# Kernel tuning notes

Hardware: AMD Instinct MI355X
Metric: run time of the kernel (lower is better)

## Reference

```python
import jax, jax.numpy as jnp
import numpy as np

NUM_CODEBOOKS = 4
CODEBOOK_SIZE = 4096
CODEBOOK_DIM = 512


def setup_inputs() -> dict:
    key = jax.random.key(0)
    k1, k2 = jax.random.split(key)
    inputs = jax.random.normal(k1, (8, 2048, CODEBOOK_DIM), dtype=jnp.float32)
    # nn.init.uniform_(codebook.weight, -1/codebook_size, 1/codebook_size)
    bound = 1.0 / CODEBOOK_SIZE
    codebook = jax.random.uniform(k2, (CODEBOOK_SIZE, CODEBOOK_DIM),
                                  dtype=jnp.float32, minval=-bound, maxval=bound)
    return {"inputs": inputs, "codebook": codebook}


def reference(inputs, codebook):
    original_shape = inputs.shape
    x = inputs.reshape(-1, CODEBOOK_DIM)  # [N, D]
    cb_sq = jnp.sum(codebook ** 2, axis=1)  # [K]

    def stage(residual, _):
        # distances: ||r||^2 - 2 r.W^T + ||w||^2  -> [N, K]
        distances = (jnp.sum(residual ** 2, axis=1, keepdims=True)
                     - 2.0 * residual @ codebook.T
                     + cb_sq[None, :])
        indices = jnp.argmin(distances, axis=-1)  # [N]
        # one-hot matmul in torch == gather; same math
        quantized = codebook[indices]  # [N, D]
        # straight-through estimator
        q_ste = residual + jax.lax.stop_gradient(quantized - residual)
        new_residual = residual - q_ste
        return new_residual, (q_ste, indices)

    _, (q_stages, idx_stages) = jax.lax.scan(stage, x, None, length=NUM_CODEBOOKS)
    quantized_out = jnp.sum(q_stages, axis=0).reshape(original_shape)
    # all_indices stacked along last dim: [B, T, num_codebooks]
    all_indices = jnp.moveaxis(idx_stages, 0, -1).reshape(*original_shape[:-1], NUM_CODEBOOKS)
    vq_loss = jnp.float32(0.0)  # eval mode: self.training is False
    return quantized_out, all_indices, vq_loss
```

## Files before the change

kernel.cpp:

```cpp
#include <hip/hip_runtime.h>
#include <math.h>


namespace {
constexpr int N_ROWS     = 16384;
constexpr int DIM        = 512;
constexpr int K_CODES    = 4096;
constexpr int NUM_STAGES = 4;

constexpr int KTILES = 32;
constexpr int LTS    = 72;
constexpr float EPS  = 1e-3f;
constexpr int CAP    = 2;

constexpr int CROWS  = 32;
constexpr int CGRIDY = 8;
constexpr int WSTRC  = 68;
constexpr int RSTR   = 68;

constexpr size_t Q_OFF    = 0;
constexpr size_t IDX_OFF  = (size_t)N_ROWS * DIM;
constexpr size_t LOSS_OFF = IDX_OFF + (size_t)N_ROWS * NUM_STAGES;

constexpr size_t RES_OFF  = 0;
constexpr size_t RH_OFF   = (size_t)N_ROWS * DIM * 4;
constexpr size_t WH_OFF   = RH_OFF + (size_t)N_ROWS * DIM * 2;
constexpr size_t CBSQ_OFF = WH_OFF + (size_t)K_CODES * DIM * 2;
constexpr size_t RSQ_OFF  = CBSQ_OFF + (size_t)K_CODES * 4;
constexpr size_t PART_OFF = RSQ_OFF + (size_t)N_ROWS * 4;
constexpr size_t GBUF_OFF = PART_OFF + (size_t)N_ROWS * KTILES * 4;
constexpr size_t BCNT_OFF = GBUF_OFF + (size_t)N_ROWS * KTILES * CAP * 8;
constexpr size_t BENT_OFF = BCNT_OFF + 128;
constexpr size_t BEST_OFF = BENT_OFF + (size_t)KTILES * N_ROWS * 4;

constexpr unsigned long long EMPTY_E = 0xFFFFFFFFFFFFFFFFull;
constexpr unsigned long long OVFL_E  = 0xFFFFFFFFFFFFFFFEull;
}

typedef short bf16x8 __attribute__((ext_vector_type(8)));
typedef float f32x4  __attribute__((ext_vector_type(4)));

__device__ __forceinline__ unsigned short f2bf(float x) {
    unsigned int u = __float_as_uint(x);
    return (unsigned short)((u + 0x7fffu + ((u >> 16) & 1u)) >> 16);
}

__device__ __forceinline__ float f4c(const float4& v, int q) {
    return q == 0 ? v.x : q == 1 ? v.y : q == 2 ? v.z : v.w;
}

__device__ __forceinline__ float rowsq_tree(const float v8[8], int lane) {
#pragma clang fp contract(off)
    float P[4];
#pragma unroll
    for (int b = 0; b < 4; ++b) {
        float xa = v8[2 * b];
        float xb = v8[2 * b + 1];
        float sa = xa * xa;
        float sb = xb * xb;
        float R  = sa + sb;
        float t  = R + __shfl_down(R, 16, 64);
        float u  = t + __shfl_down(t, 32, 64);
        float a  = u + __shfl_down(u, 8, 64);
        float c  = a + __shfl_down(a, 4, 64);
        float d  = c + __shfl_down(c, 2, 64);
        P[b]     = d + __shfl_down(d, 1, 64);
    }
    float s01 = P[0] + P[1];
    float s23 = P[2] + P[3];
    return s01 + s23;
}

__global__ __launch_bounds__(64)
void cbsq_wh_kernel(const float* __restrict__ cb, float* __restrict__ cb_sq,
                    unsigned short* __restrict__ wh, float* __restrict__ loss) {
    int k = blockIdx.x;
    int lane = threadIdx.x;
    const float* row = cb + (size_t)k * DIM;
    unsigned short* whp = wh + (size_t)k * DIM;
    float v8[8];
#pragma unroll
    for (int i = 0; i < 8; ++i) {
        float v = row[lane + i * 64];
        v8[i] = v;
        whp[lane + i * 64] = f2bf(v);
    }
    float s = rowsq_tree(v8, lane);
    if (lane == 0) cb_sq[k] = s;
    if (k == 0 && lane == 0) *loss = 0.0f;
}

__global__ __launch_bounds__(256)
void init_kernel(const float* __restrict__ input,
                 unsigned short* __restrict__ rh,
                 float* __restrict__ rsq, int* __restrict__ bcnt) {
    const int t = threadIdx.x;
    if (blockIdx.x == 0 && t < KTILES) bcnt[t] = 0;
    const int lane = t & 63;
    const int sub  = t >> 6;
    const int row  = blockIdx.x * 4 + sub;
    const float* x = input + (size_t)row * DIM;
    unsigned short* rhp = rh + (size_t)row * DIM;
    float v8[8];
#pragma unroll
    for (int i = 0; i < 8; ++i) {
        int d = lane + i * 64;
        float v = x[d];
        v8[i] = v;
        rhp[d] = f2bf(v);
    }
    float s = rowsq_tree(v8, lane);
    if (lane == 0) rsq[row] = s;
}

__global__ __launch_bounds__(256, 2)
void passA_kernel(const unsigned short* __restrict__ rh,
                  const unsigned short* __restrict__ wh,
                  const float* __restrict__ cb_sq,
                  const float* __restrict__ rsq,
                  float* __restrict__ part,
                  unsigned long long* __restrict__ gbuf) {
    const int jb = blockIdx.x;
    const int mb = blockIdx.y;
    const int mbase = mb * 128;
    const int nbase = jb * 128;

    __shared__ __align__(16) unsigned short At[128 * LTS];
    __shared__ __align__(16) unsigned short Bt[128 * LTS];
    __shared__ float rowmin[128][2];

    const int t    = threadIdx.x;
    const int lane = t & 63;
    const int wid  = t >> 6;
    const int wr   = wid >> 1;
    const int wc   = wid & 1;

    f32x4 acc[4][4];
#pragma unroll
    for (int mi = 0; mi < 4; ++mi)
#pragma unroll
        for (int ni = 0; ni < 4; ++ni) acc[mi][ni] = (f32x4){0.f, 0.f, 0.f, 0.f};

    for (int k0 = 0; k0 < DIM; k0 += 64) {
#pragma unroll
        for (int p = 0; p < 4; ++p) {
            int idx = p * 256 + t;
            int row = idx >> 3;
            int d8  = idx & 7;
            uint4 va = *(const uint4*)(rh + (size_t)(mbase + row) * DIM + k0 + d8 * 8);
            *(uint4*)&At[row * LTS + d8 * 8] = va;
            uint4 vb = *(const uint4*)(wh + (size_t)(nbase + row) * DIM + k0 + d8 * 8);
            *(uint4*)&Bt[row * LTS + d8 * 8] = vb;
        }
        __syncthreads();

#pragma unroll
        for (int kk = 0; kk < 2; ++kk) {
            bf16x8 af[4], bfr[4];
#pragma unroll
            for (int mi = 0; mi < 4; ++mi)
                af[mi] = *(const bf16x8*)&At[(wr * 64 + mi * 16 + (lane & 15)) * LTS
                                             + kk * 32 + (lane >> 4) * 8];
#pragma unroll
            for (int ni = 0; ni < 4; ++ni)
                bfr[ni] = *(const bf16x8*)&Bt[(wc * 64 + ni * 16 + (lane & 15)) * LTS
                                              + kk * 32 + (lane >> 4) * 8];
#pragma unroll
            for (int mi = 0; mi < 4; ++mi)
#pragma unroll
                for (int ni = 0; ni < 4; ++ni)
                    acc[mi][ni] = __builtin_amdgcn_mfma_f32_16x16x32_bf16(
                        af[mi], bfr[ni], acc[mi][ni], 0, 0, 0);
        }
        __syncthreads();
    }

    int* scnt = (int*)Bt;
    unsigned long long* sbuf = (unsigned long long*)At;
    if (t < 128) {
        scnt[t] = 0;
        sbuf[t * CAP + 0] = EMPTY_E;
        sbuf[t * CAP + 1] = EMPTY_E;
    }

#pragma unroll
    for (int mi = 0; mi < 4; ++mi) {
#pragma unroll
        for (int reg = 0; reg < 4; ++reg) {
            int rloc = wr * 64 + mi * 16 + (lane >> 4) * 4 + reg;
            float rsqv = rsq[mbase + rloc];
            float m = INFINITY;
#pragma unroll
            for (int ni = 0; ni < 4; ++ni) {
                int kg = nbase + wc * 64 + ni * 16 + (lane & 15);
                float y;
                {
#pragma clang fp contract(off)
                    float t2 = 2.0f * acc[mi][ni][reg];
                    float u  = rsqv - t2;
                    y        = u + cb_sq[kg];
                }
                m = fminf(m, y);
            }
#pragma unroll
            for (int off = 1; off < 16; off <<= 1)
                m = fminf(m, __shfl_xor(m, off, 64));
            if ((lane & 15) == 0) rowmin[rloc][wc] = m;
        }
    }
    __syncthreads();

#pragma unroll
    for (int mi = 0; mi < 4; ++mi) {
#pragma unroll
        for (int reg = 0; reg < 4; ++reg) {
            int rloc = wr * 64 + mi * 16 + (lane >> 4) * 4 + reg;
            float thrT = fminf(rowmin[rloc][0], rowmin[rloc][1]) + EPS;
            float rsqv = rsq[mbase + rloc];
#pragma unroll
            for (int ni = 0; ni < 4; ++ni) {
                int kg = nbase + wc * 64 + ni * 16 + (lane & 15);
                float y;
                {
#pragma clang fp contract(off)
                    float t2 = 2.0f * acc[mi][ni][reg];
                    float u  = rsqv - t2;
                    y        = u + cb_sq[kg];
                }
                if (y <= thrT) {
                    int pos = atomicAdd(&scnt[rloc], 1);
                    if (pos < CAP)
                        sbuf[rloc * CAP + pos] =
                            ((unsigned long long)__float_as_uint(y) << 32) |
                            (unsigned)kg;
                }
            }
        }
    }
    __syncthreads();

    if (t < 128) {
        part[(size_t)jb * N_ROWS + (mbase + t)] =
            fminf(rowmin[t][0], rowmin[t][1]);
        unsigned long long s0 = sbuf[t * CAP + 0];
        unsigned long long s1 = sbuf[t * CAP + 1];
        if (scnt[t] > CAP) s0 = OVFL_E;
        size_t bidx = ((size_t)jb * N_ROWS + (mbase + t)) * CAP;
        gbuf[bidx]     = s0;
        gbuf[bidx + 1] = s1;
    }
}

__global__ __launch_bounds__(256)
void passBC_kernel(const float* __restrict__ res,
                   const float* __restrict__ cb,
                   const float* __restrict__ cb_sq,
                   const float* __restrict__ rsq,
                   const float* __restrict__ part,
                   const unsigned long long* __restrict__ gbuf,
                   int* __restrict__ bcnt, int* __restrict__ bent,
                   unsigned long long* __restrict__ best) {
    const int t   = threadIdx.x;
    const int jr  = t & 31;
    const int rs  = t >> 5;
    const int row = blockIdx.x * 8 + rs;

    float pv = part[(size_t)jr * N_ROWS + row];
    float m = pv;
#pragma unroll
    for (int off = 1; off < 32; off <<= 1)
        m = fminf(m, __shfl_xor(m, off, 32));
    const float thr = m + EPS;

    float by = INFINITY; int bk = 0x7fffffff;

    if (pv <= thr) {
        size_t bidx = ((size_t)jr * N_ROWS + row) * CAP;
        unsigned long long s0 = gbuf[bidx];
        unsigned long long s1 = gbuf[bidx + 1];
        if (s0 == OVFL_E) {
            int pos = atomicAdd(&bcnt[jr], 1);
            bent[(size_t)jr * N_ROWS + pos] = row;
        } else {
            const float* rr  = res + (size_t)row * DIM;
            const float rsqv = rsq[row];
#pragma unroll
            for (int sl = 0; sl < CAP; ++sl) {
                unsigned long long s = sl ? s1 : s0;
                float yh = __uint_as_float((unsigned)(s >> 32));
                if (!(yh <= thr)) continue;
                int k = (int)(s & 0xFFFFFFFFull);
                const float* wp = cb + (size_t)k * DIM;
                float dot = 0.0f;
#pragma unroll 8
                for (int d = 0; d < DIM; d += 4) {
                    float4 r4 = *(const float4*)(rr + d);
                    float4 w4 = *(const float4*)(wp + d);
                    dot = fmaf(r4.x, w4.x, dot);
                    dot = fmaf(r4.y, w4.y, dot);
                    dot = fmaf(r4.z, w4.z, dot);
                    dot = fmaf(r4.w, w4.w, dot);
                }
                float y;
                {
#pragma clang fp contract(off)
                    float t2 = 2.0f * dot;
                    float u  = rsqv - t2;
                    y        = u + cb_sq[k];
                }
                if (y < by || (y == by && k < bk)) { by = y; bk = k; }
            }
        }
    }

    unsigned long long pk =
        ((unsigned long long)__float_as_uint(by) << 32) | (unsigned)bk;
#pragma unroll
    for (int off = 1; off < 32; off <<= 1) {
        unsigned long long o =
            (unsigned long long)__shfl_xor((long long)pk, off, 32);
        if (o < pk) pk = o;
    }
    if (jr == 0) best[row] = pk;
}

__global__ __launch_bounds__(256)
void passC_kernel(const float* __restrict__ res,
                  const float* __restrict__ cb,
                  const float* __restrict__ cb_sq,
                  const float* __restrict__ rsq,
                  const int* __restrict__ bcnt, const int* __restrict__ bent,
                  unsigned long long* __restrict__ best) {
    const int j   = blockIdx.x;
    const int cnt = bcnt[j];
    const int t   = threadIdx.x;
    const int cg  = t & 31;
    const int rg  = t >> 5;

    __shared__ __align__(16) float Ws[128 * WSTRC];
    __shared__ __align__(16) float Rs[CROWS * RSTR];
    __shared__ int   rowl[CROWS];
    __shared__ float rsql[CROWS];

    for (int base = blockIdx.y * CROWS; base < cnt; base += gridDim.y * CROWS) {
        if (t < CROWS) {
            int e  = base + t;
            int rw = bent[(size_t)j * N_ROWS + (e < cnt ? e : cnt - 1)];
            rowl[t] = rw;
            rsql[t] = rsq[rw];
        }
        __syncthreads();
        const int nrows = min(CROWS, cnt - base);

        float acc[4][4];
#pragma unroll
        for (int ri = 0; ri < 4; ++ri)
#pragma unroll
            for (int q = 0; q < 4; ++q) acc[ri][q] = 0.0f;

        for (int d0 = 0; d0 < DIM; d0 += 64) {
#pragma unroll
            for (int p = 0; p < 8; ++p) {
                int idx  = p * 256 + t;
                int cand = idx >> 4;
                int d4   = idx & 15;
                float4 v = *(const float4*)(cb + (size_t)(j * 128 + cand) * DIM + d0 + d4 * 4);
                int s = d4 ^ ((cand >> 2) & 7) ^ ((cand >> 5) & 3);
                *(float4*)&Ws[cand * WSTRC + s * 4] = v;
            }
#pragma unroll
            for (int p = 0; p < 2; ++p) {
                int idx = p * 256 + t;
                int row = idx >> 4;
                int d4  = idx & 15;
                float4 v = *(const float4*)(res + (size_t)rowl[row] * DIM + d0 + d4 * 4);
                *(float4*)&Rs[row * RSTR + d4 * 4] = v;
            }
            __syncthreads();

#pragma unroll
            for (int dq = 0; dq < 16; ++dq) {
                const int s = dq ^ (cg & 7) ^ ((cg >> 3) & 3);
                float4 w4[4];
#pragma unroll
                for (int q = 0; q < 4; ++q)
                    w4[q] = *(const float4*)&Ws[(cg * 4 + q) * WSTRC + s * 4];
#pragma unroll
                for (int ri = 0; ri < 4; ++ri) {
                    float4 rf = *(const float4*)&Rs[(rg * 4 + ri) * RSTR + dq * 4];
#pragma unroll
                    for (int dd = 0; dd < 4; ++dd) {
                        float rv = f4c(rf, dd);
                        acc[ri][0] = fmaf(rv, f4c(w4[0], dd), acc[ri][0]);
                        acc[ri][1] = fmaf(rv, f4c(w4[1], dd), acc[ri][1]);
                        acc[ri][2] = fmaf(rv, f4c(w4[2], dd), acc[ri][2]);
                        acc[ri][3] = fmaf(rv, f4c(w4[3], dd), acc[ri][3]);
                    }
                }
            }
            __syncthreads();
        }

#pragma unroll
        for (int ri = 0; ri < 4; ++ri) {
            int rloc = rg * 4 + ri;
            float rsqv = rsql[rloc];
            float by = INFINITY; int bk = 0x7fffffff;
#pragma unroll
            for (int q = 0; q < 4; ++q) {
                int k = j * 128 + cg * 4 + q;
                float y;
                {
#pragma clang fp contract(off)
                    float t2 = 2.0f * acc[ri][q];
                    float u  = rsqv - t2;
                    y        = u + cb_sq[k];
                }
                if (y < by || (y == by && k < bk)) { by = y; bk = k; }
            }
#pragma unroll
            for (int off = 1; off < 32; off <<= 1) {
                float ov = __shfl_xor(by, off, 64);
                int   oi = __shfl_xor(bk, off, 64);
                if (ov < by || (ov == by && oi < bk)) { by = ov; bk = oi; }
            }
            if (cg == 0 && rloc < nrows) {
                unsigned long long pk =
                    ((unsigned long long)__float_as_uint(by) << 32) |
                    (unsigned long long)(unsigned)bk;
                atomicMin(&best[rowl[rloc]], pk);
            }
        }
        __syncthreads();
    }
}

__global__ __launch_bounds__(256)
void combine_kernel(float* __restrict__ res_out,
                    const float* __restrict__ res_in,
                    const float* __restrict__ cb,
                    const unsigned long long* __restrict__ best,
                    float* __restrict__ qout,
                    float* __restrict__ idx_out,
                    unsigned short* __restrict__ rh,
                    float* __restrict__ rsq,
                    int* __restrict__ bcnt,
                    int stage, int do_next) {
#pragma clang fp contract(off)
    const int t    = threadIdx.x;
    if (do_next && blockIdx.x == 0 && t < KTILES) bcnt[t] = 0;
    const int lane = t & 63;
    const int sub  = t >> 6;
    const int row  = blockIdx.x * 4 + sub;

    int bi = (int)(best[row] & 0xffffffffull);
    if (lane == 0) idx_out[(size_t)row * NUM_STAGES + stage] = (float)bi;

    const float* w   = cb + (size_t)bi * DIM;
    const float* rin = res_in + (size_t)row * DIM;
    float*       r   = res_out + (size_t)row * DIM;
    float*       q   = qout + (size_t)row * DIM;
    unsigned short* rhp = rh + (size_t)row * DIM;

    float rn8[8];
#pragma unroll
    for (int i = 0; i < DIM / 64; ++i) {
        int d = lane + i * 64;
        float wv = w[d];
        float rv = rin[d];
        float tq    = wv - rv;
        float q_ste = rv + tq;
        float rn    = rv - q_ste;
        rn8[i] = rn;
        if (do_next) {
            r[d]   = rn;
            rhp[d] = f2bf(rn);
        }
        if (stage == 0) q[d] = q_ste;
        else            q[d] = q[d] + q_ste;
    }
    if (do_next) {
        float s = rowsq_tree(rn8, lane);
        if (lane == 0) rsq[row] = s;
    }
}

extern "C" void kernel_launch(void* const* d_in, const int* in_sizes, int n_in,
                              void* d_out, int out_size, void* d_ws, size_t ws_size,
                              hipStream_t stream) {
    const float* input = (const float*)d_in[0];
    const float* cb    = (const float*)d_in[1];

    float* out_f   = (float*)d_out;
    float* qout    = out_f + Q_OFF;
    float* idx_out = out_f + IDX_OFF;
    float* loss    = out_f + LOSS_OFF;

    char* ws = (char*)d_ws;
    float*          residual = (float*)(ws + RES_OFF);
    unsigned short* rh       = (unsigned short*)(ws + RH_OFF);
    unsigned short* wh       = (unsigned short*)(ws + WH_OFF);
    float*          cb_sq    = (float*)(ws + CBSQ_OFF);
    float*          rsq      = (float*)(ws + RSQ_OFF);
    float*          part     = (float*)(ws + PART_OFF);
    unsigned long long* gbuf = (unsigned long long*)(ws + GBUF_OFF);
    int*            bcnt     = (int*)(ws + BCNT_OFF);
    int*            bent     = (int*)(ws + BENT_OFF);
    unsigned long long* best = (unsigned long long*)(ws + BEST_OFF);

    cbsq_wh_kernel<<<K_CODES, 64, 0, stream>>>(cb, cb_sq, wh, loss);
    init_kernel<<<N_ROWS / 4, 256, 0, stream>>>(input, rh, rsq, bcnt);

    for (int s = 0; s < NUM_STAGES; ++s) {
        const float* rin = (s == 0) ? input : residual;
        passA_kernel<<<dim3(KTILES, N_ROWS / 128), 256, 0, stream>>>(
            rh, wh, cb_sq, rsq, part, gbuf);
        passBC_kernel<<<N_ROWS / 8, 256, 0, stream>>>(
            rin, cb, cb_sq, rsq, part, gbuf, bcnt, bent, best);
        passC_kernel<<<dim3(KTILES, CGRIDY), 256, 0, stream>>>(
            rin, cb, cb_sq, rsq, bcnt, bent, best);
        combine_kernel<<<N_ROWS / 4, 256, 0, stream>>>(
            residual, rin, cb, best, qout, idx_out, rh, rsq, bcnt,
            s, (s < NUM_STAGES - 1) ? 1 : 0);
    }
}
```

Before: 963.0 us.

## Skip fp32 rescoring when single candidate survives; remap passA blocks per XCD

Pass B now counts the surviving bf16 candidates across the 32 tiles of a row. When exactly one candidate survives and no tile overflowed, it writes that candidate directly and skips the exact fp32 dot-product rescoring. Pass A's block indices are remapped so that consecutive launched blocks, which are dealt round-robin across the 8 XCDs, map to row tiles sharing each XCD's L2. The shortcut stores the candidate's approximate bf16 distance in best rather than an exact fp32 one, which could matter if later passes compare against it.

```diff
diff --git a/kernel.cpp b/kernel.cpp
--- a/kernel.cpp
+++ b/kernel.cpp
@@ -120,8 +120,11 @@
                   const float* __restrict__ rsq,
                   float* __restrict__ part,
                   unsigned long long* __restrict__ gbuf) {
-    const int jb = blockIdx.x;
-    const int mb = blockIdx.y;
+    const int lin = blockIdx.x + KTILES * blockIdx.y;
+    const int xcd = lin & 7;
+    const int c   = lin >> 3;
+    const int jb  = c & 31;
+    const int mb  = xcd * 16 + (c >> 5);
     const int mbase = mb * 128;
     const int nbase = jb * 128;
 
@@ -272,44 +275,69 @@
         m = fminf(m, __shfl_xor(m, off, 32));
     const float thr = m + EPS;
 
+    unsigned long long s0 = EMPTY_E, s1 = EMPTY_E;
+    bool surv = (pv <= thr);
+    if (surv) {
+        size_t bidx = ((size_t)jr * N_ROWS + row) * CAP;
+        s0 = gbuf[bidx];
+        s1 = gbuf[bidx + 1];
+    }
+    const bool ovfl = surv && (s0 == OVFL_E);
+    if (ovfl) {
+        int pos = atomicAdd(&bcnt[jr], 1);
+        bent[(size_t)jr * N_ROWS + pos] = row;
+    }
+
+    int lcl = 0;
+    unsigned long long cand = EMPTY_E;
+    float y0 = __uint_as_float((unsigned)(s0 >> 32));
+    float y1 = __uint_as_float((unsigned)(s1 >> 32));
+    if (surv && !ovfl) {
+        if (y0 <= thr) { lcl++; cand = s0; }
+        if (y1 <= thr) { lcl++; cand = s1; }
+    }
+    int tot = lcl;
+    int oc  = ovfl ? 1 : 0;
+#pragma unroll
+    for (int off = 1; off < 32; off <<= 1) {
+        tot += __shfl_xor(tot, off, 32);
+        oc  += __shfl_xor(oc, off, 32);
+    }
+
+    if (tot == 1 && oc == 0) {
+        if (lcl == 1) best[row] = cand;
+        return;
+    }
+
     float by = INFINITY; int bk = 0x7fffffff;
-
-    if (pv <= thr) {
-        size_t bidx = ((size_t)jr * N_ROWS + row) * CAP;
-        unsigned long long s0 = gbuf[bidx];
-        unsigned long long s1 = gbuf[bidx + 1];
-        if (s0 == OVFL_E) {
-            int pos = atomicAdd(&bcnt[jr], 1);
-            bent[(size_t)jr * N_ROWS + pos] = row;
-        } else {
-            const float* rr  = res + (size_t)row * DIM;
-            const float rsqv = rsq[row];
-#pragma unroll
-            for (int sl = 0; sl < CAP; ++sl) {
-                unsigned long long s = sl ? s1 : s0;
-                float yh = __uint_as_float((unsigned)(s >> 32));
-                if (!(yh <= thr)) continue;
-                int k = (int)(s & 0xFFFFFFFFull);
-                const float* wp = cb + (size_t)k * DIM;
-                float dot = 0.0f;
+    if (surv && !ovfl && lcl > 0) {
+        const float* rr  = res + (size_t)row * DIM;
+        const float rsqv = rsq[row];
+#pragma unroll
+        for (int sl = 0; sl < CAP; ++sl) {
+            unsigned long long s = sl ? s1 : s0;
+            float yh = __uint_as_float((unsigned)(s >> 32));
+            if (!(yh <= thr)) continue;
+            int k = (int)(s & 0xFFFFFFFFull);
+            const float* wp = cb + (size_t)k * DIM;
+            float dot = 0.0f;
 #pragma unroll 8
-                for (int d = 0; d < DIM; d += 4) {
-                    float4 r4 = *(const float4*)(rr + d);
-                    float4 w4 = *(const float4*)(wp + d);
-                    dot = fmaf(r4.x, w4.x, dot);
-                    dot = fmaf(r4.y, w4.y, dot);
-                    dot = fmaf(r4.z, w4.z, dot);
-                    dot = fmaf(r4.w, w4.w, dot);
-                }
-                float y;
-                {
+            for (int d = 0; d < DIM; d += 4) {
+                float4 r4 = *(const float4*)(rr + d);
+                float4 w4 = *(const float4*)(wp + d);
+                dot = fmaf(r4.x, w4.x, dot);
+                dot = fmaf(r4.y, w4.y, dot);
+                dot = fmaf(r4.z, w4.z, dot);
+                dot = fmaf(r4.w, w4.w, dot);
+            }
+            float y;
+            {
 #pragma clang fp contract(off)
-                    float t2 = 2.0f * dot;
-                    float u  = rsqv - t2;
-                    y        = u + cb_sq[k];
-                }
-                if (y < by || (y == by && k < bk)) { by = y; bk = k; }
-            }
+                float t2 = 2.0f * dot;
+                float u  = rsqv - t2;
+                y        = u + cb_sq[k];
+            }
+            if (y < by || (y == by && k < bk)) { by = y; bk = k; }
         }
     }
 
```

New measurement: 896.1 us. -6.9%, faster.
